# Optimization experiments

Measured on AMD Instinct MI355X. Metric: run time of the kernel, lower is better.

## Reference

```python
import jax, jax.numpy as jnp
import numpy as np

KEY_DIM, VALUE_DIM, N_ACTIONS = 128, 64, 256
B, L = 32, 2048


def setup_inputs() -> dict:
    key = jax.random.key(0)
    k1, k2, k3 = jax.random.split(key, 3)
    key_vectors = jax.random.normal(k1, (B, L, KEY_DIM), dtype=jnp.float32)
    value_vectors = jax.random.normal(k2, (B, N_ACTIONS, KEY_DIM), dtype=jnp.float32)
    weights = jax.random.normal(k3, (KEY_DIM, VALUE_DIM, N_ACTIONS), dtype=jnp.float32)
    return {"key_vectors": key_vectors, "value_vectors": value_vectors, "weights": weights}


def reference(key_vectors, value_vectors, weights):
    # torch: einsum('bln,nka->bla', key, W) sums over both n (key_dim) and k (value_dim)
    scores = jnp.einsum('bln,nka->bla', key_vectors, weights)  # (B, L, A)
    # fused multiply-then-reduce over actions == batched matmul (no (B,L,A,D) intermediate)
    mem_vectors = jnp.einsum('bla,bad->bld', scores, value_vectors)  # (B, L, key_dim)
    q_values = jnp.einsum('bln,bmn->blm', key_vectors, mem_vectors)  # (B, L, L)
    return q_values
```

## Files before the change

kernel.cpp:

```cpp
#include <hip/hip_runtime.h>
#include <hip/hip_bf16.h>

#define KD 128
#define VD 64
#define NA 256
#define NB 32
#define LL 2048

typedef __attribute__((ext_vector_type(8))) short bf16x8;
typedef __attribute__((ext_vector_type(4))) float f32x4;
typedef __attribute__((ext_vector_type(8))) unsigned short u16x8;
typedef __attribute__((ext_vector_type(4))) unsigned short u16x4;

static __device__ __forceinline__ unsigned short f2bf(float x) {
  __hip_bfloat16 h = __float2bfloat16(x);
  unsigned short u;
  __builtin_memcpy(&u, &h, 2);
  return u;
}

static __device__ __forceinline__ void stage16(const void* gsrc, void* ldst) {
  __builtin_amdgcn_global_load_lds(
      (const __attribute__((address_space(1))) void*)gsrc,
      (__attribute__((address_space(3))) void*)ldst, 16, 0, 0);
}

__global__ __launch_bounds__(256) void fold_w(const float* __restrict__ W,
                                              float* __restrict__ W2) {
  const int idx = blockIdx.x * 256 + threadIdx.x;
  const int n = idx >> 8, a = idx & 255;
  const float* p = W + (long)n * (VD * NA) + a;
  float s = 0.f;
  #pragma unroll
  for (int k = 0; k < VD; ++k) s += p[k * NA];
  W2[idx] = s;
}

__global__ __launch_bounds__(128) void compute_t(const float* __restrict__ W2,
                                                 const float* __restrict__ V,
                                                 unsigned short* __restrict__ Tt) {
  const int n = threadIdx.x;
  const int d0 = blockIdx.x * 8;
  const int b = blockIdx.y;
  const float* vb = V + (long)b * NA * KD + d0;
  const float* w2p = W2 + n * NA;
  float acc[8] = {0.f, 0.f, 0.f, 0.f, 0.f, 0.f, 0.f, 0.f};
  for (int a = 0; a < NA; a += 4) {
    const float4 w = *(const float4*)(w2p + a);
    const float wq[4] = {w.x, w.y, w.z, w.w};
    #pragma unroll
    for (int q = 0; q < 4; ++q) {
      const float* vr = vb + (long)(a + q) * KD;
      #pragma unroll
      for (int j = 0; j < 8; ++j) acc[j] += wq[q] * vr[j];
    }
  }
  #pragma unroll
  for (int j = 0; j < 8; ++j)
    Tt[((long)b * KD + d0 + j) * KD + n] = f2bf(acc[j]);
}

__global__ __launch_bounds__(256) void cvt_key(const float* __restrict__ in,
                                               unsigned short* __restrict__ out) {
  const long i = ((long)blockIdx.x * 256 + threadIdx.x) * 8;
  const float4 f0 = *(const float4*)(in + i);
  const float4 f1 = *(const float4*)(in + i + 4);
  u16x8 r;
  r[0] = f2bf(f0.x); r[1] = f2bf(f0.y); r[2] = f2bf(f0.z); r[3] = f2bf(f0.w);
  r[4] = f2bf(f1.x); r[5] = f2bf(f1.y); r[6] = f2bf(f1.z); r[7] = f2bf(f1.w);
  *(u16x8*)(out + i) = r;
}

__global__ __launch_bounds__(512, 2) void gemm_q(const unsigned short* __restrict__ A,
                                                 const unsigned short* __restrict__ Tt,
                                                 float* __restrict__ C) {
  __shared__ unsigned short ldsB[32768];
  __shared__ unsigned short ldsA0[16384];
  __shared__ unsigned short ldsA1[16384];

  const int lg = (blockIdx.x & 7) * 32 + (blockIdx.x >> 3);
  const int nt = lg & 7;
  const int b = lg >> 3;

  const int tid = threadIdx.x;
  const int lane = tid & 63, w = tid >> 6;
  const int l15 = lane & 15, lhi = lane >> 4;
  const int wrM = w >> 2;
  const int wcN = w & 3;

  const unsigned short* gAb = A + (long)b * LL * KD;
  const unsigned short* gT = Tt + (long)b * KD * KD;
  const unsigned short* gChunk = gAb + (long)nt * 256 * KD;

  #pragma unroll
  for (int i = 0; i < 4; ++i) {
    const int addr = i * 8192 + tid * 16;
    const int row = addr >> 8;
    const int src = addr ^ ((row & 7) << 4);
    stage16((const char*)gT + src, (char*)ldsB + addr);
  }
  #pragma unroll
  for (int i = 0; i < 8; ++i) {
    const int addr = i * 8192 + tid * 16;
    const int row = addr >> 8;
    const int src = addr ^ ((row & 7) << 4);
    char* dst = (addr < 32768) ? ((char*)ldsA0 + addr) : ((char*)ldsA1 + addr - 32768);
    stage16((const char*)gChunk + src, dst);
  }
  asm volatile("s_waitcnt vmcnt(0)" ::: "memory");
  __builtin_amdgcn_s_barrier();
  __builtin_amdgcn_sched_barrier(0);

  f32x4 pacc[2][8];
  #pragma unroll
  for (int i = 0; i < 2; ++i)
    #pragma unroll
    for (int j = 0; j < 8; ++j) pacc[i][j] = f32x4{0.f, 0.f, 0.f, 0.f};

  #pragma unroll
  for (int ks = 0; ks < 4; ++ks) {
    const int kb = (ks * 32 + lhi * 8) * 2;
    bf16x8 av[2], bv[8];
    #pragma unroll
    for (int rf = 0; rf < 2; ++rf) {
      const int row = w * 32 + rf * 16 + l15;
      const int byte = (row * 256 + kb) ^ ((row & 7) << 4);
      av[rf] = (row < 128)
          ? *(const bf16x8*)((const char*)ldsA0 + byte)
          : *(const bf16x8*)((const char*)ldsA1 + (byte - 32768));
    }
    #pragma unroll
    for (int df = 0; df < 8; ++df) {
      const int row = df * 16 + l15;
      const int byte = (row * 256 + kb) ^ ((row & 7) << 4);
      bv[df] = *(const bf16x8*)((const char*)ldsB + byte);
    }
    #pragma unroll
    for (int rf = 0; rf < 2; ++rf)
      #pragma unroll
      for (int df = 0; df < 8; ++df)
        pacc[rf][df] = __builtin_amdgcn_mfma_f32_16x16x32_bf16(bv[df], av[rf],
                                                               pacc[rf][df], 0, 0, 0);
  }
  asm volatile("s_waitcnt lgkmcnt(0)" ::: "memory");
  __builtin_amdgcn_sched_barrier(0);
  __builtin_amdgcn_s_barrier();
  __builtin_amdgcn_sched_barrier(0);

  #pragma unroll
  for (int i = 0; i < 4; ++i) {
    const int addr = i * 8192 + tid * 16;
    const int row = addr >> 8;
    const int src = addr ^ ((row & 7) << 4);
    stage16((const char*)gAb + src, (char*)ldsA0 + addr);
  }
  __builtin_amdgcn_sched_barrier(0);
  #pragma unroll
  for (int rf = 0; rf < 2; ++rf)
    #pragma unroll
    for (int df = 0; df < 8; ++df) {
      const int row = w * 32 + rf * 16 + l15;
      const int d = df * 16 + lhi * 4;
      u16x4 v;
      #pragma unroll
      for (int i = 0; i < 4; ++i) v[i] = f2bf(pacc[rf][df][i]);
      const int byte = (row * 256 + d * 2) ^ ((row & 7) << 4);
      *(u16x4*)((char*)ldsB + byte) = v;
    }
  asm volatile("s_waitcnt vmcnt(0) lgkmcnt(0)" ::: "memory");
  __builtin_amdgcn_sched_barrier(0);
  __builtin_amdgcn_s_barrier();
  __builtin_amdgcn_sched_barrier(0);

  const int col0 = nt * 256 + wcN * 64;

  auto gen = [&](int mt, const unsigned short* abuf, unsigned short* nbuf) {
    if (mt < 15) {
      const char* gA = (const char*)(gAb + (long)(mt + 1) * 128 * KD);
      #pragma unroll
      for (int i = 0; i < 4; ++i) {
        const int addr = i * 8192 + tid * 16;
        const int row = addr >> 8;
        const int src = addr ^ ((row & 7) << 4);
        stage16(gA + src, (char*)nbuf + addr);
      }
    }
    __builtin_amdgcn_sched_barrier(0);

    f32x4 acc[4][4];
    #pragma unroll
    for (int i = 0; i < 4; ++i)
      #pragma unroll
      for (int j = 0; j < 4; ++j) acc[i][j] = f32x4{0.f, 0.f, 0.f, 0.f};

    #pragma unroll
    for (int ks = 0; ks < 4; ++ks) {
      const int kb = (ks * 32 + lhi * 8) * 2;
      bf16x8 av[4], bv[4];
      #pragma unroll
      for (int mf = 0; mf < 4; ++mf) {
        const int row = wrM * 64 + mf * 16 + l15;
        const int byte = (row * 256 + kb) ^ ((row & 7) << 4);
        av[mf] = *(const bf16x8*)((const char*)abuf + byte);
      }
      #pragma unroll
      for (int nf = 0; nf < 4; ++nf) {
        const int row = wcN * 64 + nf * 16 + l15;
        const int byte = (row * 256 + kb) ^ ((row & 7) << 4);
        bv[nf] = *(const bf16x8*)((const char*)ldsB + byte);
      }
      #pragma unroll
      for (int mf = 0; mf < 4; ++mf)
        #pragma unroll
        for (int nf = 0; nf < 4; ++nf)
          acc[mf][nf] = __builtin_amdgcn_mfma_f32_16x16x32_bf16(bv[nf], av[mf],
                                                                acc[mf][nf], 0, 0, 0);
    }

    const long row0 = (long)b * LL + mt * 128 + wrM * 64;
    #pragma unroll
    for (int mf = 0; mf < 4; ++mf)
      #pragma unroll
      for (int nf = 0; nf < 4; ++nf) {
        const long r = row0 + mf * 16 + l15;
        const int c = col0 + nf * 16 + lhi * 4;
        *(f32x4*)(C + r * LL + c) = acc[mf][nf];
      }

    if (mt < 15) {
      asm volatile("s_waitcnt vmcnt(16)" ::: "memory");
      __builtin_amdgcn_sched_barrier(0);
      __builtin_amdgcn_s_barrier();
      __builtin_amdgcn_sched_barrier(0);
    }
  };

  #pragma unroll 1
  for (int mt2 = 0; mt2 < 8; ++mt2) {
    gen(2 * mt2, ldsA0, ldsA1);
    gen(2 * mt2 + 1, ldsA1, ldsA0);
  }
}

extern "C" void kernel_launch(void* const* d_in, const int* in_sizes, int n_in,
                              void* d_out, int out_size, void* d_ws, size_t ws_size,
                              hipStream_t stream) {
  const float* key = (const float*)d_in[0];
  const float* val = (const float*)d_in[1];
  const float* wts = (const float*)d_in[2];
  float* out = (float*)d_out;

  char* ws = (char*)d_ws;
  float* W2 = (float*)ws;
  unsigned short* Tt = (unsigned short*)(ws + 131072);
  unsigned short* keyB = (unsigned short*)(ws + 131072 + 1048576);

  fold_w<<<128, 256, 0, stream>>>(wts, W2);
  cvt_key<<<4096, 256, 0, stream>>>(key, keyB);
  compute_t<<<dim3(16, NB), 128, 0, stream>>>(W2, val, Tt);
  gemm_q<<<8 * NB, 512, 0, stream>>>(keyB, Tt, out);
}
```

Measured before the change: 153.8 us.

## Fuse fp32-to-bf16 key conversion into the GEMM kernel's load path

Removes the separate cvt_key kernel and its bf16 workspace buffer. The GEMM now loads fp32 key tiles into registers, converts them to bf16 and writes them to swizzled LDS, replacing the direct global-to-LDS loads. This saves a kernel launch and a full write-then-read of the bf16 key copy. In exchange each block reads twice as many bytes of key data (which other blocks also re-read), needs more VGPRs for staging, and adds conversion and LDS-store work inside the pipelined loop.

```diff
diff --git a/kernel.cpp b/kernel.cpp
--- a/kernel.cpp
+++ b/kernel.cpp
@@ -23,6 +23,13 @@
   __builtin_amdgcn_global_load_lds(
       (const __attribute__((address_space(1))) void*)gsrc,
       (__attribute__((address_space(3))) void*)ldst, 16, 0, 0);
+}
+
+static __device__ __forceinline__ u16x8 cvt8(const float4 f0, const float4 f1) {
+  u16x8 v;
+  v[0] = f2bf(f0.x); v[1] = f2bf(f0.y); v[2] = f2bf(f0.z); v[3] = f2bf(f0.w);
+  v[4] = f2bf(f1.x); v[5] = f2bf(f1.y); v[6] = f2bf(f1.z); v[7] = f2bf(f1.w);
+  return v;
 }
 
 __global__ __launch_bounds__(256) void fold_w(const float* __restrict__ W,
@@ -60,18 +67,7 @@
     Tt[((long)b * KD + d0 + j) * KD + n] = f2bf(acc[j]);
 }
 
-__global__ __launch_bounds__(256) void cvt_key(const float* __restrict__ in,
-                                               unsigned short* __restrict__ out) {
-  const long i = ((long)blockIdx.x * 256 + threadIdx.x) * 8;
-  const float4 f0 = *(const float4*)(in + i);
-  const float4 f1 = *(const float4*)(in + i + 4);
-  u16x8 r;
-  r[0] = f2bf(f0.x); r[1] = f2bf(f0.y); r[2] = f2bf(f0.z); r[3] = f2bf(f0.w);
-  r[4] = f2bf(f1.x); r[5] = f2bf(f1.y); r[6] = f2bf(f1.z); r[7] = f2bf(f1.w);
-  *(u16x8*)(out + i) = r;
-}
-
-__global__ __launch_bounds__(512, 2) void gemm_q(const unsigned short* __restrict__ A,
+__global__ __launch_bounds__(512, 2) void gemm_q(const float* __restrict__ key,
                                                  const unsigned short* __restrict__ Tt,
                                                  float* __restrict__ C) {
   __shared__ unsigned short ldsB[32768];
@@ -88,9 +84,9 @@
   const int wrM = w >> 2;
   const int wcN = w & 3;
 
-  const unsigned short* gAb = A + (long)b * LL * KD;
+  const float* gK = key + (long)b * LL * KD;
   const unsigned short* gT = Tt + (long)b * KD * KD;
-  const unsigned short* gChunk = gAb + (long)nt * 256 * KD;
+  const float* gChunk = gK + (long)nt * 256 * KD;
 
   #pragma unroll
   for (int i = 0; i < 4; ++i) {
@@ -99,15 +95,28 @@
     const int src = addr ^ ((row & 7) << 4);
     stage16((const char*)gT + src, (char*)ldsB + addr);
   }
-  #pragma unroll
-  for (int i = 0; i < 8; ++i) {
-    const int addr = i * 8192 + tid * 16;
-    const int row = addr >> 8;
-    const int src = addr ^ ((row & 7) << 4);
-    char* dst = (addr < 32768) ? ((char*)ldsA0 + addr) : ((char*)ldsA1 + addr - 32768);
-    stage16((const char*)gChunk + src, dst);
-  }
-  asm volatile("s_waitcnt vmcnt(0)" ::: "memory");
+  {
+    float4 cf[8][2];
+    #pragma unroll
+    for (int it = 0; it < 8; ++it) {
+      const int idx = it * 512 + tid;
+      const int row = idx >> 4, c8 = idx & 15;
+      const float* p = gChunk + (long)row * KD + c8 * 8;
+      cf[it][0] = *(const float4*)p;
+      cf[it][1] = *(const float4*)(p + 4);
+    }
+    #pragma unroll
+    for (int it = 0; it < 8; ++it) {
+      const int idx = it * 512 + tid;
+      const int row = idx >> 4, c8 = idx & 15;
+      const u16x8 v = cvt8(cf[it][0], cf[it][1]);
+      const int byte = (row * 256 + c8 * 16) ^ ((row & 7) << 4);
+      if (byte < 32768) *(u16x8*)((char*)ldsA0 + byte) = v;
+      else              *(u16x8*)((char*)ldsA1 + byte - 32768) = v;
+    }
+  }
+  asm volatile("s_waitcnt vmcnt(0) lgkmcnt(0)" ::: "memory");
+  __builtin_amdgcn_sched_barrier(0);
   __builtin_amdgcn_s_barrier();
   __builtin_amdgcn_sched_barrier(0);
 
@@ -147,12 +156,14 @@
   __builtin_amdgcn_s_barrier();
   __builtin_amdgcn_sched_barrier(0);
 
-  #pragma unroll
-  for (int i = 0; i < 4; ++i) {
-    const int addr = i * 8192 + tid * 16;
-    const int row = addr >> 8;
-    const int src = addr ^ ((row & 7) << 4);
-    stage16((const char*)gAb + src, (char*)ldsA0 + addr);
+  float4 af[4][2];
+  #pragma unroll
+  for (int it = 0; it < 4; ++it) {
+    const int idx = it * 512 + tid;
+    const int row = idx >> 4, c8 = idx & 15;
+    const float* p = gK + (long)row * KD + c8 * 8;
+    af[it][0] = *(const float4*)p;
+    af[it][1] = *(const float4*)(p + 4);
   }
   __builtin_amdgcn_sched_barrier(0);
   #pragma unroll
@@ -167,7 +178,17 @@
       const int byte = (row * 256 + d * 2) ^ ((row & 7) << 4);
       *(u16x4*)((char*)ldsB + byte) = v;
     }
-  asm volatile("s_waitcnt vmcnt(0) lgkmcnt(0)" ::: "memory");
+  asm volatile("s_waitcnt vmcnt(0)" ::: "memory");
+  __builtin_amdgcn_sched_barrier(0);
+  #pragma unroll
+  for (int it = 0; it < 4; ++it) {
+    const int idx = it * 512 + tid;
+    const int row = idx >> 4, c8 = idx & 15;
+    const u16x8 v = cvt8(af[it][0], af[it][1]);
+    const int byte = (row * 256 + c8 * 16) ^ ((row & 7) << 4);
+    *(u16x8*)((char*)ldsA0 + byte) = v;
+  }
+  asm volatile("s_waitcnt lgkmcnt(0)" ::: "memory");
   __builtin_amdgcn_sched_barrier(0);
   __builtin_amdgcn_s_barrier();
   __builtin_amdgcn_sched_barrier(0);
@@ -175,14 +196,16 @@
   const int col0 = nt * 256 + wcN * 64;
 
   auto gen = [&](int mt, const unsigned short* abuf, unsigned short* nbuf) {
+    float4 nf4[4][2];
     if (mt < 15) {
-      const char* gA = (const char*)(gAb + (long)(mt + 1) * 128 * KD);
-      #pragma unroll
-      for (int i = 0; i < 4; ++i) {
-        const int addr = i * 8192 + tid * 16;
-        const int row = addr >> 8;
-        const int src = addr ^ ((row & 7) << 4);
-        stage16(gA + src, (char*)nbuf + addr);
+      const float* gA = gK + (long)(mt + 1) * 128 * KD;
+      #pragma unroll
+      for (int it = 0; it < 4; ++it) {
+        const int idx = it * 512 + tid;
+        const int row = idx >> 4, c8 = idx & 15;
+        const float* p = gA + (long)row * KD + c8 * 8;
+        nf4[it][0] = *(const float4*)p;
+        nf4[it][1] = *(const float4*)(p + 4);
       }
     }
     __builtin_amdgcn_sched_barrier(0);
@@ -229,6 +252,16 @@
 
     if (mt < 15) {
       asm volatile("s_waitcnt vmcnt(16)" ::: "memory");
+      __builtin_amdgcn_sched_barrier(0);
+      #pragma unroll
+      for (int it = 0; it < 4; ++it) {
+        const int idx = it * 512 + tid;
+        const int row = idx >> 4, c8 = idx & 15;
+        const u16x8 v = cvt8(nf4[it][0], nf4[it][1]);
+        const int byte = (row * 256 + c8 * 16) ^ ((row & 7) << 4);
+        *(u16x8*)((char*)nbuf + byte) = v;
+      }
+      asm volatile("s_waitcnt lgkmcnt(0)" ::: "memory");
       __builtin_amdgcn_sched_barrier(0);
       __builtin_amdgcn_s_barrier();
       __builtin_amdgcn_sched_barrier(0);
@@ -253,10 +286,8 @@
   char* ws = (char*)d_ws;
   float* W2 = (float*)ws;
   unsigned short* Tt = (unsigned short*)(ws + 131072);
-  unsigned short* keyB = (unsigned short*)(ws + 131072 + 1048576);
 
   fold_w<<<128, 256, 0, stream>>>(wts, W2);
-  cvt_key<<<4096, 256, 0, stream>>>(key, keyB);
   compute_t<<<dim3(16, NB), 128, 0, stream>>>(W2, val, Tt);
-  gemm_q<<<8 * NB, 512, 0, stream>>>(keyB, Tt, out);
-}
+  gemm_q<<<8 * NB, 512, 0, stream>>>(key, Tt, out);
+}
```

Result: slower. 157.9 us (+2.7%).
